# Kernel optimization log

Hardware: AMD Instinct MI355X
Metric: run time of the kernel (lower is better)

Reference implementation:

```python
import jax, jax.numpy as jnp
import numpy as np

IOU_THR = 0.8
SCORE_THR = 0.7
INNER_THR = 0.5
EPS = 1e-8


def setup_inputs() -> dict:
    key = jax.random.key(0)
    k1, k2 = jax.random.split(key)
    N, H, W = 1024, 256, 256
    masks = (jax.random.uniform(k1, (N, H, W)) < 0.15).astype(jnp.float32)
    scores = jax.random.uniform(k2, (N,), dtype=jnp.float32)
    return {"masks": masks, "scores": scores}


def reference(masks, scores):
    N = masks.shape[0]
    # sort by score descending (torch: scores.sort(0, descending=True))
    order = jnp.argsort(-scores)
    s = scores[order]
    flat = masks[order].reshape(N, -1).astype(jnp.float32)  # [N, H*W]
    area = jnp.sum(flat, axis=1)                            # [N]

    inter = flat @ flat.T                                   # [N, N]
    union = area[None, :] + area[:, None] - inter
    iou = inter / (union + EPS)
    ratio_i = inter / (area[:, None] + EPS)
    ratio_j = inter / (area[None, :] + EPS)
    vals = 1.0 - ratio_j * ratio_i

    cond1 = (ratio_i < 0.5) & (ratio_j >= 0.85)
    cond2 = (ratio_i >= 0.85) & (ratio_j < 0.5)
    # inner_iou_matrix[cond1] = vals[cond1]
    inner = jnp.where(cond1, vals, 0.0)
    # inner_iou_matrix.T[cond2] = vals[cond2]  =>  inner[j,i] = vals[i,j] where cond2[i,j]
    inner = jnp.where(cond2.T, vals.T, inner)

    triu1 = jnp.triu(jnp.ones((N, N), dtype=bool), k=1)
    tril1 = jnp.tril(jnp.ones((N, N), dtype=bool), k=1)  # note diagonal=1, matches torch.tril(., 1)

    iou_max = jnp.max(jnp.where(triu1, iou, 0.0), axis=0)
    inner_max_u = jnp.max(jnp.where(triu1, inner, 0.0), axis=0)
    inner_max_l = jnp.max(jnp.where(tril1, inner, 0.0), axis=0)

    keep = iou_max <= IOU_THR
    keep_conf = s > SCORE_THR
    # fallback: if no mask passes score threshold, keep top-3 by score
    _, top3 = jax.lax.top_k(s, 3)
    fallback = jnp.zeros((N,), dtype=bool).at[top3].set(True)
    keep_conf = jnp.where(jnp.any(keep_conf), keep_conf, fallback)

    keep = keep & keep_conf & (inner_max_u <= 1.0 - INNER_THR) & (inner_max_l <= 1.0 - INNER_THR)
    # torch returns idx[keep] (dynamic shape); we return (order, keep) which is equivalent info
    return order, keep
```

## Files before the change

### kernel.cpp

```cpp
#include <hip/hip_runtime.h>


#define N_MASKS 1024
#define HW 65536
#define WPR 2048
#define NT 8
#define NPAIRS 36
#define KQ 16

typedef float vfloat4 __attribute__((ext_vector_type(4)));
typedef int v4i __attribute__((ext_vector_type(4)));
typedef int v16i __attribute__((ext_vector_type(16)));

__device__ __forceinline__ void tile_from_pair(int p, int& I, int& J) {
    int rem = p, i = 0;
    while (rem >= NT - i) { rem -= NT - i; ++i; }
    I = i; J = i + rem;
}

__device__ __forceinline__ v4i expand16(unsigned word, int sh) {
    v4i r;
    r[0] = (int)((((word >> (sh + 0))  & 0xFu) * 0x00204081u) & 0x01010101u);
    r[1] = (int)((((word >> (sh + 4))  & 0xFu) * 0x00204081u) & 0x01010101u);
    r[2] = (int)((((word >> (sh + 8))  & 0xFu) * 0x00204081u) & 0x01010101u);
    r[3] = (int)((((word >> (sh + 12)) & 0xFu) * 0x00204081u) & 0x01010101u);
    return r;
}

__global__ __launch_bounds__(128) void sort_kernel(const float* __restrict__ scores,
                                                   int* __restrict__ order,
                                                   float* __restrict__ ssort,
                                                   int* __restrict__ out_order,
                                                   float* __restrict__ area,
                                                   unsigned* __restrict__ ioumax,
                                                   unsigned* __restrict__ innu,
                                                   unsigned* __restrict__ innl) {
    __shared__ float s[N_MASKS];
    const int t = threadIdx.x;
    for (int k = t; k < N_MASKS; k += 128) s[k] = scores[k];
    __syncthreads();
    const int i = blockIdx.x * 128 + t;
    const float si = s[i];
    int rank = 0;
    #pragma unroll 8
    for (int j = 0; j < N_MASKS; ++j) {
        const float sj = s[j];
        rank += (int)((sj > si) || (sj == si && j < i));
    }
    order[rank] = i;
    ssort[rank] = si;
    out_order[rank] = i;
    area[i] = 0.0f;
    ioumax[i] = 0u; innu[i] = 0u; innl[i] = 0u;
}

__global__ __launch_bounds__(256, 4) void pack_kernel(const float* __restrict__ masks,
                                                      const int* __restrict__ order,
                                                      unsigned* __restrict__ packed,
                                                      float* __restrict__ area) {
    const int b = blockIdx.x;
    const int r = b >> 2, q = b & 3;
    const int src = order[r];
    const vfloat4* __restrict__ row = (const vfloat4*)(masks + (size_t)src * HW) + q * 4096;
    unsigned* __restrict__ prow = packed + (size_t)r * WPR + q * 512;
    const int t = threadIdx.x;

    vfloat4 f[16];
    #pragma unroll
    for (int k = 0; k < 16; ++k)
        f[k] = __builtin_nontemporal_load(row + k * 256 + t);

    unsigned w0 = 0u, w1 = 0u;
    #pragma unroll
    for (int k = 0; k < 8; ++k) {
        const unsigned nib0 = (unsigned)(f[k][0] != 0.0f)        | ((unsigned)(f[k][1] != 0.0f) << 1)
                            | ((unsigned)(f[k][2] != 0.0f) << 2) | ((unsigned)(f[k][3] != 0.0f) << 3);
        w0 |= nib0 << (k * 4);
        const unsigned nib1 = (unsigned)(f[k + 8][0] != 0.0f)        | ((unsigned)(f[k + 8][1] != 0.0f) << 1)
                            | ((unsigned)(f[k + 8][2] != 0.0f) << 2) | ((unsigned)(f[k + 8][3] != 0.0f) << 3);
        w1 |= nib1 << (k * 4);
    }
    prow[t] = w0;
    prow[256 + t] = w1;

    int cnt = __builtin_popcount(w0) + __builtin_popcount(w1);
    for (int off = 32; off > 0; off >>= 1) cnt += __shfl_down(cnt, off, 64);
    __shared__ int red[4];
    const int lane = t & 63, w = t >> 6;
    if (lane == 0) red[w] = cnt;
    __syncthreads();
    if (t == 0) atomicAdd(area + r, (float)(red[0] + red[1] + red[2] + red[3]));
}

__global__ __launch_bounds__(256, 3) void pair_kernel(const unsigned* __restrict__ packed,
                                                      int* __restrict__ partial) {
    const int p = blockIdx.x, kq = blockIdx.y;
    int I, J; tile_from_pair(p, I, J);
    const int A0 = I * 128, B0 = J * 128;
    const int t = threadIdx.x;
    const int wave = t >> 6, lane = t & 63, half = lane >> 5, lr = lane & 31;
    const int wr = (wave >> 1) * 64, wc = (wave & 1) * 64;

    if (I == J && wave == 2) return;

    const unsigned* __restrict__ rowA0 = packed + (size_t)(A0 + wr + lr) * WPR + kq * 128;
    const unsigned* __restrict__ rowA1 = rowA0 + 32 * WPR;
    const unsigned* __restrict__ rowB0 = packed + (size_t)(B0 + wc + lr) * WPR + kq * 128;
    const unsigned* __restrict__ rowB1 = rowB0 + 32 * WPR;
    const int sh = half * 16;

    v16i acc[2][2];
    #pragma unroll
    for (int i = 0; i < 2; ++i)
        #pragma unroll
        for (int j = 0; j < 2; ++j)
            #pragma unroll
            for (int r = 0; r < 16; ++r) acc[i][j][r] = 0;

    #pragma unroll 2
    for (int g = 0; g < 32; ++g) {
        const uint4 wa0 = *(const uint4*)(rowA0 + g * 4);
        const uint4 wa1 = *(const uint4*)(rowA1 + g * 4);
        const uint4 wb0 = *(const uint4*)(rowB0 + g * 4);
        const uint4 wb1 = *(const uint4*)(rowB1 + g * 4);
        const unsigned a0w[4] = { wa0.x, wa0.y, wa0.z, wa0.w };
        const unsigned a1w[4] = { wa1.x, wa1.y, wa1.z, wa1.w };
        const unsigned b0w[4] = { wb0.x, wb0.y, wb0.z, wb0.w };
        const unsigned b1w[4] = { wb1.x, wb1.y, wb1.z, wb1.w };
        #pragma unroll
        for (int w = 0; w < 4; ++w) {
            const v4i a0 = expand16(a0w[w], sh);
            const v4i a1 = expand16(a1w[w], sh);
            const v4i b0 = expand16(b0w[w], sh);
            const v4i b1 = expand16(b1w[w], sh);
            acc[0][0] = __builtin_amdgcn_mfma_i32_32x32x32_i8(a0, b0, acc[0][0], 0, 0, 0);
            acc[0][1] = __builtin_amdgcn_mfma_i32_32x32x32_i8(a0, b1, acc[0][1], 0, 0, 0);
            acc[1][0] = __builtin_amdgcn_mfma_i32_32x32x32_i8(a1, b0, acc[1][0], 0, 0, 0);
            acc[1][1] = __builtin_amdgcn_mfma_i32_32x32x32_i8(a1, b1, acc[1][1], 0, 0, 0);
        }
    }

    int* __restrict__ outp = partial + ((size_t)kq * NPAIRS + p) * 16384;
    #pragma unroll
    for (int i = 0; i < 2; ++i)
        #pragma unroll
        for (int j = 0; j < 2; ++j)
            #pragma unroll
            for (int reg = 0; reg < 16; ++reg) {
                const int m = wr + i * 32 + (reg & 3) + 8 * (reg >> 2) + 4 * half;
                const int n = wc + j * 32 + lr;
                outp[m * 128 + n] = acc[i][j][reg];
            }
}

__global__ __launch_bounds__(256) void combine_kernel(const unsigned* __restrict__ partial,
                                                      const float* __restrict__ area,
                                                      unsigned* __restrict__ ioumax,
                                                      unsigned* __restrict__ innu,
                                                      unsigned* __restrict__ innl) {
    __shared__ unsigned redI[128], redU[128], redLB[128], redLA[8];
    __shared__ float aB[128];

    const int p = blockIdx.x, rg = blockIdx.y;
    int I, J; tile_from_pair(p, I, J);
    const int A0 = I * 128, B0 = J * 128;
    const int t = threadIdx.x;
    if (t < 128) { redI[t] = 0u; redU[t] = 0u; redLB[t] = 0u; aB[t] = area[B0 + t]; }
    if (t < 8) redLA[t] = 0u;
    __syncthreads();

    const int row = rg * 8 + (t >> 5);
    const int col = (t & 31) * 4;
    const int a = A0 + row;
    const float fa = area[a];

    unsigned sx = 0, sy = 0, sz = 0, sw = 0;
    #pragma unroll
    for (int kq = 0; kq < KQ; ++kq) {
        const uint4 v = *(const uint4*)(partial + ((size_t)kq * NPAIRS + p) * 16384 + row * 128 + col);
        sx += v.x; sy += v.y; sz += v.z; sw += v.w;
    }
    const unsigned sums[4] = { sx, sy, sz, sw };

    float mLA = 0.0f;
    #pragma unroll
    for (int j = 0; j < 4; ++j) {
        const int b = B0 + col + j;
        if (a > b) continue;
        const float inter = (float)sums[j];
        const float fb = aB[col + j];
        const float uni = (fb + fa) - inter;
        const float iou = inter / (uni + 1e-8f);
        const float ra = inter / (fa + 1e-8f);
        const float rb = inter / (fb + 1e-8f);
        const float v = __fsub_rn(1.0f, __fmul_rn(rb, ra));
        const float iab = (ra < 0.5f && rb >= 0.85f) ? v : 0.0f;
        const float iba = (rb < 0.5f && ra >= 0.85f) ? v : 0.0f;
        if (a < b) {
            atomicMax(&redI[col + j], __float_as_uint(iou));
            atomicMax(&redU[col + j], __float_as_uint(iab));
            mLA = fmaxf(mLA, iba);
        }
        if (a == b - 1) atomicMax(&redLB[col + j], __float_as_uint(iab));
    }
    atomicMax(&redLA[t >> 5], __float_as_uint(mLA));
    __syncthreads();
    if (t < 128) {
        atomicMax(&ioumax[B0 + t], redI[t]);
        atomicMax(&innu[B0 + t], redU[t]);
        atomicMax(&innl[B0 + t], redLB[t]);
    }
    if (t < 8) atomicMax(&innl[A0 + rg * 8 + t], redLA[t]);
}

__global__ __launch_bounds__(256) void keep_kernel(const float* __restrict__ ssort,
                                                   const unsigned* __restrict__ ioumax,
                                                   const unsigned* __restrict__ innu,
                                                   const unsigned* __restrict__ innl,
                                                   int* __restrict__ out_keep) {
    const int r = blockIdx.x * 256 + threadIdx.x;
    const float s0 = ssort[0];
    const bool conf = (s0 > 0.7f) ? (ssort[r] > 0.7f) : (r < 3);
    const bool keep = (__uint_as_float(ioumax[r]) <= 0.8f) && conf &&
                      (__uint_as_float(innu[r]) <= 0.5f) &&
                      (__uint_as_float(innl[r]) <= 0.5f);
    out_keep[r] = keep ? 1 : 0;
}

extern "C" void kernel_launch(void* const* d_in, const int* in_sizes, int n_in,
                              void* d_out, int out_size, void* d_ws, size_t ws_size,
                              hipStream_t stream) {
    const float* masks  = (const float*)d_in[0];
    const float* scores = (const float*)d_in[1];
    int* out = (int*)d_out;

    unsigned* packed  = (unsigned*)d_ws;
    unsigned* partial = packed + (size_t)N_MASKS * WPR;
    unsigned* tail    = partial + (size_t)KQ * NPAIRS * 16384;
    int*      order   = (int*)tail;
    float*    ssort   = (float*)(order + N_MASKS);
    float*    area    = (float*)(ssort + N_MASKS);
    unsigned* ioumax  = (unsigned*)(area + N_MASKS);
    unsigned* innu    = ioumax + N_MASKS;
    unsigned* innl    = innu + N_MASKS;

    sort_kernel<<<8, 128, 0, stream>>>(scores, order, ssort, out, area, ioumax, innu, innl);
    pack_kernel<<<4096, 256, 0, stream>>>(masks, order, packed, area);
    pair_kernel<<<dim3(NPAIRS, KQ), 256, 0, stream>>>(packed, (int*)partial);
    combine_kernel<<<dim3(NPAIRS, KQ), 256, 0, stream>>>(partial, area, ioumax, innu, innl);
    keep_kernel<<<4, 256, 0, stream>>>(ssort, ioumax, innu, innl, out + N_MASKS);
}
```

Baseline: 429.5 us.

## Fuse sort into pack kernel and keep into combine via last-block counter

The score sort now runs inside the first four blocks of the pack kernel, and masks are packed in their original order. The pair and combine kernels gather rows through the order array instead of the pack kernel permuting them. Per-quarter areas are written directly, which replaces the float atomicAdd, and the keep step runs in the last-finishing combine block detected with a global atomic counter. This removes two kernel launches and the serial dependency between sort and pack, at the cost of indirect row addressing in the MFMA kernel and extra fence and atomic work.

Result: slower. 453.2 us (+5.5%).

```diff
diff --git a/kernel.cpp b/kernel.cpp
--- a/kernel.cpp
+++ b/kernel.cpp
@@ -1,7 +1,7 @@
 #include <hip/hip_runtime.h>
 
 
-#define N_MASKS 1024
+#define NM 1024
 #define HW 65536
 #define WPR 2048
 #define NT 8
@@ -27,41 +27,23 @@
     return r;
 }
 
-__global__ __launch_bounds__(128) void sort_kernel(const float* __restrict__ scores,
-                                                   int* __restrict__ order,
-                                                   float* __restrict__ ssort,
-                                                   int* __restrict__ out_order,
-                                                   float* __restrict__ area,
-                                                   unsigned* __restrict__ ioumax,
-                                                   unsigned* __restrict__ innu,
-                                                   unsigned* __restrict__ innl) {
-    __shared__ float s[N_MASKS];
-    const int t = threadIdx.x;
-    for (int k = t; k < N_MASKS; k += 128) s[k] = scores[k];
-    __syncthreads();
-    const int i = blockIdx.x * 128 + t;
-    const float si = s[i];
-    int rank = 0;
-    #pragma unroll 8
-    for (int j = 0; j < N_MASKS; ++j) {
-        const float sj = s[j];
-        rank += (int)((sj > si) || (sj == si && j < i));
-    }
-    order[rank] = i;
-    ssort[rank] = si;
-    out_order[rank] = i;
-    area[i] = 0.0f;
-    ioumax[i] = 0u; innu[i] = 0u; innl[i] = 0u;
-}
-
-__global__ __launch_bounds__(256, 4) void pack_kernel(const float* __restrict__ masks,
-                                                      const int* __restrict__ order,
-                                                      unsigned* __restrict__ packed,
-                                                      float* __restrict__ area) {
+__global__ __launch_bounds__(256) void pack_init_kernel(const float* __restrict__ masks,
+                                                        const float* __restrict__ scores,
+                                                        unsigned* __restrict__ packed,
+                                                        unsigned* __restrict__ areaQ,
+                                                        int* __restrict__ order,
+                                                        float* __restrict__ ssort,
+                                                        int* __restrict__ out_order,
+                                                        unsigned* __restrict__ ioumax,
+                                                        unsigned* __restrict__ innu,
+                                                        unsigned* __restrict__ innl,
+                                                        unsigned* __restrict__ counter) {
+    __shared__ int red[4];
+    __shared__ float s[NM];
+
     const int b = blockIdx.x;
     const int r = b >> 2, q = b & 3;
-    const int src = order[r];
-    const vfloat4* __restrict__ row = (const vfloat4*)(masks + (size_t)src * HW) + q * 4096;
+    const vfloat4* __restrict__ row = (const vfloat4*)(masks + (size_t)r * HW) + q * 4096;
     unsigned* __restrict__ prow = packed + (size_t)r * WPR + q * 512;
     const int t = threadIdx.x;
 
@@ -85,14 +67,32 @@
 
     int cnt = __builtin_popcount(w0) + __builtin_popcount(w1);
     for (int off = 32; off > 0; off >>= 1) cnt += __shfl_down(cnt, off, 64);
-    __shared__ int red[4];
     const int lane = t & 63, w = t >> 6;
     if (lane == 0) red[w] = cnt;
     __syncthreads();
-    if (t == 0) atomicAdd(area + r, (float)(red[0] + red[1] + red[2] + red[3]));
+    if (t == 0) areaQ[b] = (unsigned)(red[0] + red[1] + red[2] + red[3]);
+
+    if (b < 4) {
+        for (int k = t; k < NM; k += 256) s[k] = scores[k];
+        __syncthreads();
+        const int i = b * 256 + t;
+        const float si = s[i];
+        int rank = 0;
+        #pragma unroll 8
+        for (int j = 0; j < NM; ++j) {
+            const float sj = s[j];
+            rank += (int)((sj > si) || (sj == si && j < i));
+        }
+        order[rank] = i;
+        ssort[rank] = si;
+        out_order[rank] = i;
+        ioumax[i] = 0u; innu[i] = 0u; innl[i] = 0u;
+    }
+    if (b == 4 && t == 0) *counter = 0u;
 }
 
 __global__ __launch_bounds__(256, 3) void pair_kernel(const unsigned* __restrict__ packed,
+                                                      const int* __restrict__ order,
                                                       int* __restrict__ partial) {
     const int p = blockIdx.x, kq = blockIdx.y;
     int I, J; tile_from_pair(p, I, J);
@@ -103,10 +103,10 @@
 
     if (I == J && wave == 2) return;
 
-    const unsigned* __restrict__ rowA0 = packed + (size_t)(A0 + wr + lr) * WPR + kq * 128;
-    const unsigned* __restrict__ rowA1 = rowA0 + 32 * WPR;
-    const unsigned* __restrict__ rowB0 = packed + (size_t)(B0 + wc + lr) * WPR + kq * 128;
-    const unsigned* __restrict__ rowB1 = rowB0 + 32 * WPR;
+    const unsigned* __restrict__ rowA0 = packed + (size_t)order[A0 + wr + lr] * WPR + kq * 128;
+    const unsigned* __restrict__ rowA1 = packed + (size_t)order[A0 + wr + 32 + lr] * WPR + kq * 128;
+    const unsigned* __restrict__ rowB0 = packed + (size_t)order[B0 + wc + lr] * WPR + kq * 128;
+    const unsigned* __restrict__ rowB1 = packed + (size_t)order[B0 + wc + 32 + lr] * WPR + kq * 128;
     const int sh = half * 16;
 
     v16i acc[2][2];
@@ -153,26 +153,36 @@
             }
 }
 
-__global__ __launch_bounds__(256) void combine_kernel(const unsigned* __restrict__ partial,
-                                                      const float* __restrict__ area,
-                                                      unsigned* __restrict__ ioumax,
-                                                      unsigned* __restrict__ innu,
-                                                      unsigned* __restrict__ innl) {
+__global__ __launch_bounds__(256) void combine_keep_kernel(const unsigned* __restrict__ partial,
+                                                           const unsigned* __restrict__ areaQ,
+                                                           const int* __restrict__ order,
+                                                           const float* __restrict__ ssort,
+                                                           unsigned* __restrict__ ioumax,
+                                                           unsigned* __restrict__ innu,
+                                                           unsigned* __restrict__ innl,
+                                                           unsigned* __restrict__ counter,
+                                                           int* __restrict__ out_keep) {
     __shared__ unsigned redI[128], redU[128], redLB[128], redLA[8];
     __shared__ float aB[128];
+    __shared__ unsigned done;
 
     const int p = blockIdx.x, rg = blockIdx.y;
     int I, J; tile_from_pair(p, I, J);
     const int A0 = I * 128, B0 = J * 128;
     const int t = threadIdx.x;
-    if (t < 128) { redI[t] = 0u; redU[t] = 0u; redLB[t] = 0u; aB[t] = area[B0 + t]; }
+    if (t < 128) {
+        redI[t] = 0u; redU[t] = 0u; redLB[t] = 0u;
+        const int id = order[B0 + t];
+        aB[t] = (float)(areaQ[4 * id] + areaQ[4 * id + 1] + areaQ[4 * id + 2] + areaQ[4 * id + 3]);
+    }
     if (t < 8) redLA[t] = 0u;
     __syncthreads();
 
     const int row = rg * 8 + (t >> 5);
     const int col = (t & 31) * 4;
     const int a = A0 + row;
-    const float fa = area[a];
+    const int ida = order[a];
+    const float fa = (float)(areaQ[4 * ida] + areaQ[4 * ida + 1] + areaQ[4 * ida + 2] + areaQ[4 * ida + 3]);
 
     unsigned sx = 0, sy = 0, sz = 0, sw = 0;
     #pragma unroll
@@ -211,20 +221,24 @@
         atomicMax(&innl[B0 + t], redLB[t]);
     }
     if (t < 8) atomicMax(&innl[A0 + rg * 8 + t], redLA[t]);
-}
-
-__global__ __launch_bounds__(256) void keep_kernel(const float* __restrict__ ssort,
-                                                   const unsigned* __restrict__ ioumax,
-                                                   const unsigned* __restrict__ innu,
-                                                   const unsigned* __restrict__ innl,
-                                                   int* __restrict__ out_keep) {
-    const int r = blockIdx.x * 256 + threadIdx.x;
-    const float s0 = ssort[0];
-    const bool conf = (s0 > 0.7f) ? (ssort[r] > 0.7f) : (r < 3);
-    const bool keep = (__uint_as_float(ioumax[r]) <= 0.8f) && conf &&
-                      (__uint_as_float(innu[r]) <= 0.5f) &&
-                      (__uint_as_float(innl[r]) <= 0.5f);
-    out_keep[r] = keep ? 1 : 0;
+
+    __threadfence();
+    if (t == 0) done = atomicAdd(counter, 1u);
+    __syncthreads();
+    if (done == (unsigned)(NPAIRS * KQ - 1)) {
+        __threadfence();
+        const float s0 = ssort[0];
+        for (int r = t; r < NM; r += 256) {
+            const bool conf = (s0 > 0.7f) ? (ssort[r] > 0.7f) : (r < 3);
+            const unsigned vi = atomicOr(ioumax + r, 0u);
+            const unsigned vu = atomicOr(innu + r, 0u);
+            const unsigned vl = atomicOr(innl + r, 0u);
+            const bool keep = (__uint_as_float(vi) <= 0.8f) && conf &&
+                              (__uint_as_float(vu) <= 0.5f) &&
+                              (__uint_as_float(vl) <= 0.5f);
+            out_keep[r] = keep ? 1 : 0;
+        }
+    }
 }
 
 extern "C" void kernel_launch(void* const* d_in, const int* in_sizes, int n_in,
@@ -235,18 +249,20 @@
     int* out = (int*)d_out;
 
     unsigned* packed  = (unsigned*)d_ws;
-    unsigned* partial = packed + (size_t)N_MASKS * WPR;
+    unsigned* partial = packed + (size_t)NM * WPR;
     unsigned* tail    = partial + (size_t)KQ * NPAIRS * 16384;
     int*      order   = (int*)tail;
-    float*    ssort   = (float*)(order + N_MASKS);
-    float*    area    = (float*)(ssort + N_MASKS);
-    unsigned* ioumax  = (unsigned*)(area + N_MASKS);
-    unsigned* innu    = ioumax + N_MASKS;
-    unsigned* innl    = innu + N_MASKS;
-
-    sort_kernel<<<8, 128, 0, stream>>>(scores, order, ssort, out, area, ioumax, innu, innl);
-    pack_kernel<<<4096, 256, 0, stream>>>(masks, order, packed, area);
-    pair_kernel<<<dim3(NPAIRS, KQ), 256, 0, stream>>>(packed, (int*)partial);
-    combine_kernel<<<dim3(NPAIRS, KQ), 256, 0, stream>>>(partial, area, ioumax, innu, innl);
-    keep_kernel<<<4, 256, 0, stream>>>(ssort, ioumax, innu, innl, out + N_MASKS);
-}
+    float*    ssort   = (float*)(order + NM);
+    unsigned* areaQ   = (unsigned*)(ssort + NM);
+    unsigned* ioumax  = areaQ + 4 * NM;
+    unsigned* innu    = ioumax + NM;
+    unsigned* innl    = innu + NM;
+    unsigned* counter = innl + NM;
+
+    pack_init_kernel<<<4096, 256, 0, stream>>>(masks, scores, packed, areaQ, order, ssort,
+                                               out, ioumax, innu, innl, counter);
+    pair_kernel<<<dim3(NPAIRS, KQ), 256, 0, stream>>>(packed, order, (int*)partial);
+    combine_keep_kernel<<<dim3(NPAIRS, KQ), 256, 0, stream>>>(partial, areaQ, order, ssort,
+                                                              ioumax, innu, innl, counter,
+                                                              out + NM);
+}
```
